# Optimization experiments

Measured on AMD Instinct MI355X. Metric: run time of the kernel, lower is better.

The kernel has to match this reference:

```python
import jax, jax.numpy as jnp
import numpy as np

N_NODES = 100000
N_EDGES = 1600000
NEG_SLOPE = 0.2
EPS = 1e-16


def _gat_layer(x, src, dst, W, att_src, att_dst, bias, heads, out_ch):
    # x: [N, F_in]; src/dst: [E'] (self-loops already appended)
    n = x.shape[0]
    h = (x @ W).reshape(n, heads, out_ch)                      # [N, H, C]
    a_src = (h * att_src[None]).sum(-1)                        # [N, H]
    a_dst = (h * att_dst[None]).sum(-1)                        # [N, H]
    e = a_src[src] + a_dst[dst]                                # [E', H]
    e = jnp.where(e > 0, e, NEG_SLOPE * e)                     # leaky_relu
    # segment softmax over incoming edges of each dst node
    m = jax.ops.segment_max(e, dst, num_segments=n)            # [N, H]
    ex = jnp.exp(e - m[dst])                                   # [E', H]
    s = jax.ops.segment_sum(ex, dst, num_segments=n)           # [N, H]
    alpha = ex / (s[dst] + EPS)                                # [E', H]
    msg = h[src] * alpha[:, :, None]                           # [E', H, C]
    out = jax.ops.segment_sum(msg, dst, num_segments=n)        # [N, H, C]
    return out.reshape(n, heads * out_ch) + bias


def setup_inputs() -> dict:
    key = jax.random.key(0)
    ks = jax.random.split(key, 10)
    x = jax.random.normal(ks[0], (N_NODES, 165), dtype=jnp.float32)
    src = jax.random.randint(ks[1], (N_EDGES,), 0, N_NODES, dtype=jnp.int32)
    dst = jax.random.randint(ks[2], (N_EDGES,), 0, N_NODES, dtype=jnp.int32)
    glorot = lambda k, shp: jax.random.normal(k, shp, dtype=jnp.float32) * jnp.sqrt(2.0 / (shp[0] + shp[-1]))
    W1 = glorot(ks[3], (165, 256))
    att_src1 = glorot(ks[4], (4, 64))
    att_dst1 = glorot(ks[5], (4, 64))
    b1 = jnp.zeros((256,), dtype=jnp.float32)
    W2 = glorot(ks[6], (256, 2))
    att_src2 = glorot(ks[7], (1, 2))
    att_dst2 = glorot(ks[8], (1, 2))
    b2 = jnp.zeros((2,), dtype=jnp.float32)
    return {"x": x, "src": src, "dst": dst,
            "W1": W1, "att_src1": att_src1, "att_dst1": att_dst1, "b1": b1,
            "W2": W2, "att_src2": att_src2, "att_dst2": att_dst2, "b2": b2}


def reference(x, src, dst, W1, att_src1, att_dst1, b1, W2, att_src2, att_dst2, b2):
    n = x.shape[0]
    # PyG GATConv adds self-loops by default
    loops = jnp.arange(n, dtype=src.dtype)
    s = jnp.concatenate([src, loops])
    d = jnp.concatenate([dst, loops])
    h = _gat_layer(x, s, d, W1, att_src1, att_dst1, b1, heads=4, out_ch=64)
    h = jax.nn.relu(h)
    # F.dropout with training=False is identity (eval mode)
    out = _gat_layer(h, s, d, W2, att_src2, att_dst2, b2, heads=1, out_ch=2)
    return jax.nn.log_softmax(out, axis=1)
```

## Files before the change

kernel.cpp:

```cpp
#include <hip/hip_runtime.h>
#include <math.h>

#define NN 100000
#define NE 1600000
#define ET (NE + NN)
#define NEG 0.2f
#define NBLK ((NN + 255) / 256)
#define KP 192

typedef __attribute__((ext_vector_type(8))) short short8;
typedef __attribute__((ext_vector_type(4))) float floatx4;

__device__ __forceinline__ unsigned short f2bf(float f) {
    unsigned u = __float_as_uint(f);
    unsigned r = u + 0x7fffu + ((u >> 16) & 1u);
    return (unsigned short)(r >> 16);
}
__device__ __forceinline__ float bflo(unsigned x) { return __uint_as_float(x << 16); }
__device__ __forceinline__ float bfhi(unsigned x) { return __uint_as_float(x & 0xFFFF0000u); }

__global__ __launch_bounds__(192) void k_prep(const float* __restrict__ W,
                                              unsigned short* __restrict__ Wt) {
    const int n = blockIdx.x, k = threadIdx.x;
    Wt[n * KP + k] = (k < 165) ? f2bf(W[k * 256 + n]) : (unsigned short)0;
}

__global__ __launch_bounds__(256) void k_gemm1(const float* __restrict__ x,
                                               const unsigned short* __restrict__ Wt,
                                               const float* __restrict__ att_s,
                                               const float* __restrict__ att_d,
                                               unsigned short* __restrict__ h1,
                                               float* __restrict__ a_src,
                                               float* __restrict__ a_dst) {
    __shared__ __align__(16) unsigned short sh[2][32 * 200];
    unsigned* lds_p = (unsigned*)&sh[0][0];
    const int t = threadIdx.x;
    const int n0 = blockIdx.x * 32;
    for (int idx = t; idx < 32 * 35; idx += 256) {
        const int row = idx / 35, k = 165 + (idx - row * 35);
        sh[0][row * 200 + k] = 0;
        sh[1][row * 200 + k] = 0;
    }
    for (int idx = t; idx < 32 * 165; idx += 256) {
        const int row = idx / 165, k = idx - row * 165;
        const float v = x[(size_t)n0 * 165 + idx];
        const unsigned short hi = f2bf(v);
        const float r = v - __uint_as_float((unsigned)hi << 16);
        sh[0][row * 200 + k] = hi;
        sh[1][row * 200 + k] = f2bf(r);
    }
    __syncthreads();

    const int lane = t & 63, hd = t >> 6;
    const int r16 = lane & 15, quad = lane >> 4;
    floatx4 zero4 = {0.0f, 0.0f, 0.0f, 0.0f};
    floatx4 acc[2][4];
#pragma unroll
    for (int mm = 0; mm < 2; ++mm)
#pragma unroll
        for (int nn = 0; nn < 4; ++nn) acc[mm][nn] = zero4;

    for (int ks = 0; ks < 6; ++ks) {
        const int kb = ks * 32 + quad * 8;
        short8 ah0 = *(const short8*)&sh[0][(r16) * 200 + kb];
        short8 ah1 = *(const short8*)&sh[0][(16 + r16) * 200 + kb];
        short8 al0 = *(const short8*)&sh[1][(r16) * 200 + kb];
        short8 al1 = *(const short8*)&sh[1][(16 + r16) * 200 + kb];
        short8 bf[4];
#pragma unroll
        for (int nn = 0; nn < 4; ++nn)
            bf[nn] = *(const short8*)(Wt + (size_t)(hd * 64 + nn * 16 + r16) * KP + kb);
#pragma unroll
        for (int nn = 0; nn < 4; ++nn) {
            acc[0][nn] = __builtin_amdgcn_mfma_f32_16x16x32_bf16(ah0, bf[nn], acc[0][nn], 0, 0, 0);
            acc[0][nn] = __builtin_amdgcn_mfma_f32_16x16x32_bf16(al0, bf[nn], acc[0][nn], 0, 0, 0);
            acc[1][nn] = __builtin_amdgcn_mfma_f32_16x16x32_bf16(ah1, bf[nn], acc[1][nn], 0, 0, 0);
            acc[1][nn] = __builtin_amdgcn_mfma_f32_16x16x32_bf16(al1, bf[nn], acc[1][nn], 0, 0, 0);
        }
    }

    float asw[4], adw[4];
#pragma unroll
    for (int nn = 0; nn < 4; ++nn) {
        asw[nn] = att_s[hd * 64 + nn * 16 + r16];
        adw[nn] = att_d[hd * 64 + nn * 16 + r16];
    }
#pragma unroll
    for (int mm = 0; mm < 2; ++mm)
#pragma unroll
        for (int r = 0; r < 4; ++r) {
            float ps = acc[mm][0][r] * asw[0] + acc[mm][1][r] * asw[1] +
                       acc[mm][2][r] * asw[2] + acc[mm][3][r] * asw[3];
            float pd = acc[mm][0][r] * adw[0] + acc[mm][1][r] * adw[1] +
                       acc[mm][2][r] * adw[2] + acc[mm][3][r] * adw[3];
            ps += __shfl_xor(ps, 1); ps += __shfl_xor(ps, 2);
            ps += __shfl_xor(ps, 4); ps += __shfl_xor(ps, 8);
            pd += __shfl_xor(pd, 1); pd += __shfl_xor(pd, 2);
            pd += __shfl_xor(pd, 4); pd += __shfl_xor(pd, 8);
            if (r16 == 0) {
                const int node = n0 + mm * 16 + quad * 4 + r;
                a_src[node * 4 + hd] = ps;
                a_dst[node * 4 + hd] = pd;
            }
        }

    __syncthreads();
#pragma unroll
    for (int mm = 0; mm < 2; ++mm)
#pragma unroll
        for (int nn = 0; nn < 4; ++nn)
#pragma unroll
            for (int r = 0; r < 4; ++r) {
                const float v = acc[mm][nn][r];
                const float o = __shfl_xor(v, 1);
                if ((lane & 1) == 0) {
                    const unsigned pk = (unsigned)f2bf(v) | ((unsigned)f2bf(o) << 16);
                    lds_p[(mm * 16 + quad * 4 + r) * 132 + hd * 32 + nn * 8 + (r16 >> 1)] = pk;
                }
            }
    __syncthreads();
    {
        const int row = t & 31, seg = t >> 5;
        const unsigned* p = &lds_p[row * 132 + seg * 16];
        uint4 d0 = *(const uint4*)(p);
        uint4 d1 = *(const uint4*)(p + 4);
        uint4 d2 = *(const uint4*)(p + 8);
        uint4 d3 = *(const uint4*)(p + 12);
        unsigned short* hp = h1 + (size_t)(n0 + row) * 256 + seg * 32;
        *(uint4*)(hp) = d0;
        *(uint4*)(hp + 8) = d1;
        *(uint4*)(hp + 16) = d2;
        *(uint4*)(hp + 24) = d3;
    }
}

__global__ __launch_bounds__(256) void k_hist(const int* __restrict__ dst,
                                              int* __restrict__ deg, int* __restrict__ eoff) {
    const int e = blockIdx.x * 256 + threadIdx.x;
    if (e >= ET) return;
    const int d = (e < NE) ? dst[e] : (e - NE);
    eoff[e] = atomicAdd(&deg[d], 1);
}

__global__ __launch_bounds__(256) void k_scan1(const int* __restrict__ deg,
                                               int* __restrict__ excl, int* __restrict__ bsum) {
    __shared__ int sh[256];
    const int t = threadIdx.x;
    const int i = blockIdx.x * 256 + t;
    const int v = (i < NN) ? deg[i] : 0;
    sh[t] = v;
    __syncthreads();
    for (int off = 1; off < 256; off <<= 1) {
        int add = (t >= off) ? sh[t - off] : 0;
        __syncthreads();
        sh[t] += add;
        __syncthreads();
    }
    if (i < NN) excl[i] = sh[t] - v;
    if (t == 255) bsum[blockIdx.x] = sh[255];
}

__global__ __launch_bounds__(512) void k_scan2(int* __restrict__ bsum) {
    __shared__ int sh[512];
    const int t = threadIdx.x;
    const int v = (t < NBLK) ? bsum[t] : 0;
    sh[t] = v;
    __syncthreads();
    for (int off = 1; off < 512; off <<= 1) {
        int add = (t >= off) ? sh[t - off] : 0;
        __syncthreads();
        sh[t] += add;
        __syncthreads();
    }
    if (t < NBLK) bsum[t] = sh[t] - v;
}

__global__ __launch_bounds__(256) void k_scan3(const int* __restrict__ excl, const int* __restrict__ bsum,
                                               int* __restrict__ rowptr) {
    const int i = blockIdx.x * 256 + threadIdx.x;
    if (i < NN) rowptr[i] = excl[i] + bsum[blockIdx.x];
    if (i == 0) rowptr[NN] = ET;
}

__global__ __launch_bounds__(256) void k_scatter(const int* __restrict__ src, const int* __restrict__ dst,
                                                 const int* __restrict__ eoff, const int* __restrict__ rowptr,
                                                 int* __restrict__ esrc) {
    const int e = blockIdx.x * 256 + threadIdx.x;
    if (e >= ET) return;
    int s, d;
    if (e < NE) { s = src[e]; d = dst[e]; } else { s = d = e - NE; }
    esrc[rowptr[d] + eoff[e]] = s;
}

__global__ __launch_bounds__(256) void k_l1agg(const unsigned short* __restrict__ h1,
                                               const float* __restrict__ a_src,
                                               const float* __restrict__ a_dst,
                                               const int* __restrict__ rowptr,
                                               const int* __restrict__ esrc,
                                               const float* __restrict__ b1,
                                               const float* __restrict__ W2,
                                               const float* __restrict__ att_s2,
                                               const float* __restrict__ att_d2,
                                               float4* __restrict__ node2) {
    const int t = threadIdx.x;
    const int n = blockIdx.x * 4 + (t >> 6);
    const int l = t & 63;
    const int q = l >> 4;
    const int sl = l & 15;
    const int head = sl >> 2;
    const int c0 = sl * 16;
    const int el = l >> 2;
    const int hl = l & 3;
    const int beg = rowptr[n], end = rowptr[n + 1];
    const float4 ad4 = *(const float4*)&a_dst[n * 4];
    const float adh = (hl == 0) ? ad4.x : (hl == 1) ? ad4.y : (hl == 2) ? ad4.z : ad4.w;

    float ssum = 0.0f;
    float acc[16];
#pragma unroll
    for (int c = 0; c < 16; ++c) acc[c] = 0.0f;

    for (int base = beg; base < end; base += 16) {
        const int cnt = end - base;
        const int iters = (cnt < 16) ? cnt : 16;
        int sA = 0; float pA = 0.0f;
        if (el < cnt) {
            sA = esrc[base + el];
            const float a = a_src[sA * 4 + hl] + adh;
            const float e = (a > 0.0f) ? a : NEG * a;
            pA = __expf(e);
        }
#pragma unroll
        for (int jb = 0; jb < 16; jb += 4) {
            const int j = jb + q;
            const int s = __shfl(sA, j << 2);
            const float p = __shfl(pA, (j << 2) | head);
            if (j < iters) {
                ssum += p;
                const unsigned ho = ((unsigned)s << 8) + c0;
                const uint4 hv0 = *(const uint4*)(h1 + ho);
                const uint4 hv1 = *(const uint4*)(h1 + ho + 8);
                acc[0]  += p * bflo(hv0.x); acc[1]  += p * bfhi(hv0.x);
                acc[2]  += p * bflo(hv0.y); acc[3]  += p * bfhi(hv0.y);
                acc[4]  += p * bflo(hv0.z); acc[5]  += p * bfhi(hv0.z);
                acc[6]  += p * bflo(hv0.w); acc[7]  += p * bfhi(hv0.w);
                acc[8]  += p * bflo(hv1.x); acc[9]  += p * bfhi(hv1.x);
                acc[10] += p * bflo(hv1.y); acc[11] += p * bfhi(hv1.y);
                acc[12] += p * bflo(hv1.z); acc[13] += p * bfhi(hv1.z);
                acc[14] += p * bflo(hv1.w); acc[15] += p * bfhi(hv1.w);
            }
        }
    }
    ssum += __shfl_xor(ssum, 16); ssum += __shfl_xor(ssum, 32);
#pragma unroll
    for (int c = 0; c < 16; ++c) {
        acc[c] += __shfl_xor(acc[c], 16);
        acc[c] += __shfl_xor(acc[c], 32);
    }
    const float inv = 1.0f / ssum;
    float p0 = 0.0f, p1 = 0.0f;
#pragma unroll
    for (int c = 0; c < 16; ++c) {
        const float v = fmaxf(acc[c] * inv + b1[c0 + c], 0.0f);
        p0 += v * W2[(c0 + c) * 2 + 0];
        p1 += v * W2[(c0 + c) * 2 + 1];
    }
    if (q) { p0 = 0.0f; p1 = 0.0f; }
#pragma unroll
    for (int off = 32; off; off >>= 1) {
        p0 += __shfl_down(p0, off);
        p1 += __shfl_down(p1, off);
    }
    if (l == 0) {
        const float as2v = p0 * att_s2[0] + p1 * att_s2[1];
        const float ad2v = p0 * att_d2[0] + p1 * att_d2[1];
        node2[n] = make_float4(p0, p1, as2v, ad2v);
    }
}

__global__ __launch_bounds__(256) void k_l2agg(const float4* __restrict__ node2,
                                               const int* __restrict__ rowptr,
                                               const int* __restrict__ esrc,
                                               const float* __restrict__ b2,
                                               float* __restrict__ out) {
    const int t = threadIdx.x;
    const int n = blockIdx.x * 4 + (t >> 6);
    const int l = t & 63;
    const int beg = rowptr[n], end = rowptr[n + 1];
    const float adst = node2[n].w;
    float ssum = 0.0f, a0 = 0.0f, a1 = 0.0f;
    for (int idx = beg + l; idx < end; idx += 64) {
        const int s = esrc[idx];
        const float4 r = node2[s];
        const float a = r.z + adst;
        const float e = (a > 0.0f) ? a : NEG * a;
        const float p = __expf(e);
        ssum += p; a0 += p * r.x; a1 += p * r.y;
    }
#pragma unroll
    for (int off = 32; off; off >>= 1) {
        ssum += __shfl_xor(ssum, off);
        a0 += __shfl_xor(a0, off);
        a1 += __shfl_xor(a1, off);
    }
    if (l == 0) {
        const float inv = 1.0f / ssum;
        const float z0 = a0 * inv + b2[0];
        const float z1 = a1 * inv + b2[1];
        const float mz = fmaxf(z0, z1);
        const float lse = mz + __logf(__expf(z0 - mz) + __expf(z1 - mz));
        out[n * 2 + 0] = z0 - lse;
        out[n * 2 + 1] = z1 - lse;
    }
}

extern "C" void kernel_launch(void* const* d_in, const int* in_sizes, int n_in,
                              void* d_out, int out_size, void* d_ws, size_t ws_size,
                              hipStream_t stream) {
    const float* x    = (const float*)d_in[0];
    const int*   src  = (const int*)d_in[1];
    const int*   dst  = (const int*)d_in[2];
    const float* W1   = (const float*)d_in[3];
    const float* as1w = (const float*)d_in[4];
    const float* ad1w = (const float*)d_in[5];
    const float* b1   = (const float*)d_in[6];
    const float* W2   = (const float*)d_in[7];
    const float* as2w = (const float*)d_in[8];
    const float* ad2w = (const float*)d_in[9];
    const float* b2   = (const float*)d_in[10];
    float* out = (float*)d_out;

    char* w = (char*)d_ws;
    unsigned short* h1 = (unsigned short*)w; w += (size_t)NN * 256 * 2;
    unsigned short* Wt = (unsigned short*)w; w += (size_t)256 * KP * 2;
    float* a_src = (float*)w; w += (size_t)NN * 4 * 4;
    float* a_dst = (float*)w; w += (size_t)NN * 4 * 4;
    float4* node2 = (float4*)w; w += (size_t)NN * 4 * 4;
    int* deg     = (int*)w;   w += (size_t)NN * 4;
    int* eoff    = (int*)w;   w += (size_t)ET * 4;
    int* excl    = (int*)w;   w += (size_t)NN * 4;
    int* bsum    = (int*)w;   w += 2048;
    int* rowptr  = (int*)w;   w += 400016;
    int* esrc    = (int*)w;   w += (size_t)ET * 4;

    hipMemsetAsync(deg, 0, (size_t)NN * 4, stream);
    k_prep<<<256, 192, 0, stream>>>(W1, Wt);
    k_gemm1<<<NN / 32, 256, 0, stream>>>(x, Wt, as1w, ad1w, h1, a_src, a_dst);
    k_hist<<<(ET + 255) / 256, 256, 0, stream>>>(dst, deg, eoff);
    k_scan1<<<NBLK, 256, 0, stream>>>(deg, excl, bsum);
    k_scan2<<<1, 512, 0, stream>>>(bsum);
    k_scan3<<<NBLK, 256, 0, stream>>>(excl, bsum, rowptr);
    k_scatter<<<(ET + 255) / 256, 256, 0, stream>>>(src, dst, eoff, rowptr, esrc);
    k_l1agg<<<NN / 4, 256, 0, stream>>>(h1, a_src, a_dst, rowptr, esrc, b1, W2, as2w, ad2w, node2);
    k_l2agg<<<NN / 4, 256, 0, stream>>>(node2, rowptr, esrc, b2, out);
}
```

Baseline: 501.8 us.

## Fuse histogram into GEMM launch, trim l1agg loop, pack l2agg nodes per wave

The edge-degree histogram blocks are appended to the layer-1 GEMM grid, so one launch runs both independent jobs and the histogram atomics overlap the GEMM. The layer-1 aggregation inner loop now stops at the actual edge count instead of being fully unrolled to 16. The layer-2 aggregation gives each node 16 lanes instead of a whole 64-lane wavefront, so four nodes share a wave, which fits the average degree of about 17. Costs are that the fused kernel reserves GEMM-sized LDS even for histogram blocks, and the l1agg inner loop loses unrolling.

New measurement: 496.2 us. About the same (-1.1%).

```diff
diff --git a/kernel.cpp b/kernel.cpp
--- a/kernel.cpp
+++ b/kernel.cpp
@@ -7,6 +7,8 @@
 #define NEG 0.2f
 #define NBLK ((NN + 255) / 256)
 #define KP 192
+#define GEMM_BLKS (NN / 32)
+#define HIST_BLKS ((ET + 255) / 256)
 
 typedef __attribute__((ext_vector_type(8))) short short8;
 typedef __attribute__((ext_vector_type(4))) float floatx4;
@@ -25,16 +27,27 @@
     Wt[n * KP + k] = (k < 165) ? f2bf(W[k * 256 + n]) : (unsigned short)0;
 }
 
-__global__ __launch_bounds__(256) void k_gemm1(const float* __restrict__ x,
-                                               const unsigned short* __restrict__ Wt,
-                                               const float* __restrict__ att_s,
-                                               const float* __restrict__ att_d,
-                                               unsigned short* __restrict__ h1,
-                                               float* __restrict__ a_src,
-                                               float* __restrict__ a_dst) {
+__global__ __launch_bounds__(256) void k_gemmhist(const float* __restrict__ x,
+                                                  const unsigned short* __restrict__ Wt,
+                                                  const float* __restrict__ att_s,
+                                                  const float* __restrict__ att_d,
+                                                  unsigned short* __restrict__ h1,
+                                                  float* __restrict__ a_src,
+                                                  float* __restrict__ a_dst,
+                                                  const int* __restrict__ dst,
+                                                  int* __restrict__ deg,
+                                                  int* __restrict__ eoff) {
+    const int t = threadIdx.x;
+    if (blockIdx.x >= GEMM_BLKS) {
+        const int e = (blockIdx.x - GEMM_BLKS) * 256 + t;
+        if (e < ET) {
+            const int d = (e < NE) ? dst[e] : (e - NE);
+            eoff[e] = atomicAdd(&deg[d], 1);
+        }
+        return;
+    }
     __shared__ __align__(16) unsigned short sh[2][32 * 200];
     unsigned* lds_p = (unsigned*)&sh[0][0];
-    const int t = threadIdx.x;
     const int n0 = blockIdx.x * 32;
     for (int idx = t; idx < 32 * 35; idx += 256) {
         const int row = idx / 35, k = 165 + (idx - row * 35);
@@ -134,14 +147,6 @@
     }
 }
 
-__global__ __launch_bounds__(256) void k_hist(const int* __restrict__ dst,
-                                              int* __restrict__ deg, int* __restrict__ eoff) {
-    const int e = blockIdx.x * 256 + threadIdx.x;
-    if (e >= ET) return;
-    const int d = (e < NE) ? dst[e] : (e - NE);
-    eoff[e] = atomicAdd(&deg[d], 1);
-}
-
 __global__ __launch_bounds__(256) void k_scan1(const int* __restrict__ deg,
                                                int* __restrict__ excl, int* __restrict__ bsum) {
     __shared__ int sh[256];
@@ -230,8 +235,7 @@
             const float e = (a > 0.0f) ? a : NEG * a;
             pA = __expf(e);
         }
-#pragma unroll
-        for (int jb = 0; jb < 16; jb += 4) {
+        for (int jb = 0; jb < iters; jb += 4) {
             const int j = jb + q;
             const int s = __shfl(sA, j << 2);
             const float p = __shfl(pA, (j << 2) | head);
@@ -284,12 +288,14 @@
                                                const float* __restrict__ b2,
                                                float* __restrict__ out) {
     const int t = threadIdx.x;
-    const int n = blockIdx.x * 4 + (t >> 6);
     const int l = t & 63;
+    const int g = l >> 4;
+    const int i = l & 15;
+    const int n = blockIdx.x * 16 + (t >> 6) * 4 + g;
     const int beg = rowptr[n], end = rowptr[n + 1];
     const float adst = node2[n].w;
     float ssum = 0.0f, a0 = 0.0f, a1 = 0.0f;
-    for (int idx = beg + l; idx < end; idx += 64) {
+    for (int idx = beg + i; idx < end; idx += 16) {
         const int s = esrc[idx];
         const float4 r = node2[s];
         const float a = r.z + adst;
@@ -298,12 +304,12 @@
         ssum += p; a0 += p * r.x; a1 += p * r.y;
     }
 #pragma unroll
-    for (int off = 32; off; off >>= 1) {
+    for (int off = 8; off; off >>= 1) {
         ssum += __shfl_xor(ssum, off);
         a0 += __shfl_xor(a0, off);
         a1 += __shfl_xor(a1, off);
     }
-    if (l == 0) {
+    if (i == 0) {
         const float inv = 1.0f / ssum;
         const float z0 = a0 * inv + b2[0];
         const float z1 = a1 * inv + b2[1];
@@ -345,12 +351,12 @@
 
     hipMemsetAsync(deg, 0, (size_t)NN * 4, stream);
     k_prep<<<256, 192, 0, stream>>>(W1, Wt);
-    k_gemm1<<<NN / 32, 256, 0, stream>>>(x, Wt, as1w, ad1w, h1, a_src, a_dst);
-    k_hist<<<(ET + 255) / 256, 256, 0, stream>>>(dst, deg, eoff);
+    k_gemmhist<<<GEMM_BLKS + HIST_BLKS, 256, 0, stream>>>(x, Wt, as1w, ad1w, h1, a_src, a_dst,
+                                                          dst, deg, eoff);
     k_scan1<<<NBLK, 256, 0, stream>>>(deg, excl, bsum);
     k_scan2<<<1, 512, 0, stream>>>(bsum);
     k_scan3<<<NBLK, 256, 0, stream>>>(excl, bsum, rowptr);
     k_scatter<<<(ET + 255) / 256, 256, 0, stream>>>(src, dst, eoff, rowptr, esrc);
     k_l1agg<<<NN / 4, 256, 0, stream>>>(h1, a_src, a_dst, rowptr, esrc, b1, W2, as2w, ad2w, node2);
-    k_l2agg<<<NN / 4, 256, 0, stream>>>(node2, rowptr, esrc, b2, out);
-}
+    k_l2agg<<<NN / 16, 256, 0, stream>>>(node2, rowptr, esrc, b2, out);
+}
```
